# Kernel tuning notes

Hardware: AMD Instinct MI355X
Metric: run time of the kernel (lower is better)

The kernel has to match this reference:

```python
import jax, jax.numpy as jnp
import numpy as np

VOCAB, HIDDEN, LAYERS = 128, 1024, 2
B, T = 128, 512


def setup_inputs() -> dict:
    key = jax.random.key(0)
    ks = jax.random.split(key, 8)
    s0 = 1.0 / np.sqrt(HIDDEN)
    x = jax.random.normal(ks[0], (B, T, VOCAB), dtype=jnp.float32)
    h = jnp.zeros((LAYERS, B, HIDDEN), dtype=jnp.float32)
    c = jnp.zeros((LAYERS, B, HIDDEN), dtype=jnp.float32)
    # LSTM params, gate order (i, f, g, o) concatenated along last dim (4H)
    Wx0 = jax.random.uniform(ks[1], (VOCAB, 4 * HIDDEN), jnp.float32, -s0, s0)
    Wh0 = jax.random.uniform(ks[2], (HIDDEN, 4 * HIDDEN), jnp.float32, -s0, s0)
    b0 = jax.random.uniform(ks[3], (4 * HIDDEN,), jnp.float32, -s0, s0)
    Wx1 = jax.random.uniform(ks[4], (HIDDEN, 4 * HIDDEN), jnp.float32, -s0, s0)
    Wh1 = jax.random.uniform(ks[5], (HIDDEN, 4 * HIDDEN), jnp.float32, -s0, s0)
    b1 = jax.random.uniform(ks[6], (4 * HIDDEN,), jnp.float32, -s0, s0)
    return {"x": x, "h": h, "c": c, "Wx0": Wx0, "Wh0": Wh0, "b0": b0,
            "Wx1": Wx1, "Wh1": Wh1, "b1": b1}


def _lstm_cell(inp, h_prev, c_prev, Wx, Wh, b):
    gates = inp @ Wx + h_prev @ Wh + b            # (B, 4H)
    i, f, g, o = jnp.split(gates, 4, axis=-1)
    i = jax.nn.sigmoid(i)
    f = jax.nn.sigmoid(f)
    g = jnp.tanh(g)
    o = jax.nn.sigmoid(o)
    c_new = f * c_prev + i * g
    h_new = o * jnp.tanh(c_new)
    return h_new, c_new


def reference(x, h, c, Wx0, Wh0, b0, Wx1, Wh1, b1):
    layer_params = [(Wx0, Wh0, b0), (Wx1, Wh1, b1)]

    def step(carry, x_t):
        h_prev, c_prev = carry                    # each (L, B, H)
        inp = x_t                                 # (B, VOCAB)
        hs, cs = [], []
        for l, (Wx, Wh, b) in enumerate(layer_params):
            h_new, c_new = _lstm_cell(inp, h_prev[l], c_prev[l], Wx, Wh, b)
            hs.append(h_new)
            cs.append(c_new)
            inp = h_new
        return (jnp.stack(hs), jnp.stack(cs)), hs[-1]

    xs = jnp.swapaxes(x, 0, 1)                    # (T, B, VOCAB)
    (h_f, c_f), outs = jax.lax.scan(step, (h, c), xs)
    outs = jnp.swapaxes(outs, 0, 1)               # (B, T, H)
    return outs, h_f, c_f
```

## Files before the change

kernel.cpp:

```cpp
#include <hip/hip_runtime.h>

#define VV 128
#define HH 1024
#define BB 128
#define TT 512
#define G4 4096
#define BTH ((size_t)BB * TT * HH)
#define HPAR (4 * 64 * 512)

typedef __attribute__((ext_vector_type(8))) short bf16x8;
typedef __attribute__((ext_vector_type(16))) float f32x16;

__device__ __forceinline__ short f2bf(float f) {
  unsigned u = __float_as_uint(f);
  u = (u + 0x7fffu + ((u >> 16) & 1u)) >> 16;
  return (short)u;
}

__device__ __forceinline__ float fsig(float x) {
  x = fminf(fmaxf(x, -30.f), 30.f);
  float e = __expf(-x);
  return 1.f / (1.f + e);
}
__device__ __forceinline__ float ftanh(float x) {
  x = fminf(fmaxf(x, -15.f), 15.f);
  float e = __expf(-2.f * x);
  return (1.f - e) / (1.f + e);
}


__global__ void conv_x(const float* __restrict__ x, short* __restrict__ xp) {
  const int n = TT * 4 * 8 * 512;
  for (int i = blockIdx.x * blockDim.x + threadIdx.x; i < n; i += gridDim.x * blockDim.x) {
    int e = i & 7, lane = (i >> 3) & 63, kc = (i >> 9) & 7, rb = (i >> 12) & 3, t = i >> 14;
    int row = rb * 32 + (lane & 31);
    int v = kc * 16 + ((lane >> 5) << 3) + e;
    xp[i] = f2bf(x[((size_t)row * TT + t) * VV + v]);
  }
}

__global__ void init_state(const float* __restrict__ h,
                           short* __restrict__ h0p, short* __restrict__ h1p) {
  const int n = 2 * HPAR;
  for (int i = blockIdx.x * blockDim.x + threadIdx.x; i < n; i += gridDim.x * blockDim.x) {
    int inner = i & (HPAR - 1);
    int l = i >> 17;
    int e = i & 7, lane = (i >> 3) & 63, kc = (i >> 9) & 63, rb = (i >> 15) & 3;
    int row = rb * 32 + (lane & 31);
    int j = kc * 16 + ((lane >> 5) << 3) + e;
    short hb = f2bf(h[((size_t)l * BB + row) * HH + j]);
    (l ? h1p : h0p)[HPAR + inner] = hb;
  }
}

__global__ void pack_w(const float* __restrict__ Wx0, const float* __restrict__ Wh0,
                       const float* __restrict__ Wx1, const float* __restrict__ Wh1,
                       short* __restrict__ wp0, short* __restrict__ wp1) {
  const int n0 = 128 * 72 * 512;
  const int n1 = 128 * 128 * 512;
  for (int i = blockIdx.x * blockDim.x + threadIdx.x; i < n0 + n1; i += gridDim.x * blockDim.x) {
    if (i < n0) {
      int cu = i / (72 * 512);
      int rem = i - cu * (72 * 512);
      int kc = rem >> 9, le = rem & 511;
      int lane = le >> 3, e = le & 7;
      int k = kc * 16 + ((lane >> 5) << 3) + e;
      int cl = lane & 31;
      int gcol = (cl >> 3) * HH + cu * 8 + (cl & 7);
      float f = (k < VV) ? Wx0[(size_t)k * G4 + gcol] : Wh0[(size_t)(k - VV) * G4 + gcol];
      wp0[i] = f2bf(f);
    } else {
      int j = i - n0;
      int cu = j >> 16;
      int rem = j & 65535;
      int kc = rem >> 9, le = rem & 511;
      int lane = le >> 3, e = le & 7;
      int k = kc * 16 + ((lane >> 5) << 3) + e;
      int cl = lane & 31;
      int gcol = (cl >> 3) * HH + cu * 8 + (cl & 7);
      float f = (k < HH) ? Wx1[(size_t)k * G4 + gcol] : Wh1[(size_t)(k - HH) * G4 + gcol];
      wp1[j] = f2bf(f);
    }
  }
}

__global__ void pack_b(const float* __restrict__ b0, const float* __restrict__ b1,
                       float* __restrict__ bp, unsigned* __restrict__ slots) {
  int i = blockIdx.x * blockDim.x + threadIdx.x;
  if (i < 2 * 128 * 32) {
    int l = i >> 12;
    int cu = (i >> 5) & 127;
    int cc = i & 31;
    const float* b = l ? b1 : b0;
    bp[i] = b[(cc >> 3) * HH + cu * 8 + (cc & 7)];
  }
  if (i < 512) slots[i] = 0u;
}


template <int NCH>
__device__ __forceinline__ void hgemm(f32x16* acc, const short* pa0, const short* pa1,
                                      const short* __restrict__ pb) {
  constexpr int NG = NCH / 16;
  bf16x8 A[3][16];
#pragma unroll
  for (int g = 0; g < 3; ++g) {
#pragma unroll
    for (int j = 0; j < 16; ++j) {
      const int c = g * 16 + j;
      const short* ap = (c < 64) ? (pa0 + c * 512) : (pa1 + (c - 64) * 512);
      asm volatile("global_load_dwordx4 %0, %1, off sc0 sc1" : "=v"(A[g][j]) : "v"(ap));
    }
  }
#pragma unroll
  for (int g = 0; g < NG; ++g) {
    const int rem = NG - 1 - g;
    if (rem >= 2)      asm volatile("s_waitcnt vmcnt(32)" ::: "memory");
    else if (rem == 1) asm volatile("s_waitcnt vmcnt(16)" ::: "memory");
    else               asm volatile("s_waitcnt vmcnt(0)" ::: "memory");
#pragma unroll
    for (int j = 0; j < 16; ++j)
      asm volatile("" : "+v"(A[g % 3][j]));
#pragma unroll
    for (int j = 0; j < 16; ++j) {
      const int c = g * 16 + j;
      bf16x8 b = *(const bf16x8*)(pb + c * 512);
      acc[j & 3] = __builtin_amdgcn_mfma_f32_32x32x16_bf16(A[g % 3][j], b, acc[j & 3], 0, 0, 0);
    }
    if (g + 3 < NG) {
#pragma unroll
      for (int j = 0; j < 16; ++j) {
        const int c = (g + 3) * 16 + j;
        const short* ap = (c < 64) ? (pa0 + c * 512) : (pa1 + (c - 64) * 512);
        asm volatile("global_load_dwordx4 %0, %1, off sc0 sc1"
                     : "=v"(A[(g + 3) % 3][j]) : "v"(ap));
      }
    }
  }
}

__device__ __forceinline__ void xgemm(f32x16* acc, const short* __restrict__ pax,
                                      const short* __restrict__ pb) {
#pragma unroll
  for (int c = 0; c < 8; ++c) {
    bf16x8 a = *(const bf16x8*)(pax + c * 512);
    bf16x8 b = *(const bf16x8*)(pb + c * 512);
    acc[c & 3] = __builtin_amdgcn_mfma_f32_32x32x16_bf16(a, b, acc[c & 3], 0, 0, 0);
  }
}

__global__ void __launch_bounds__(256, 1) lstm_main(const short* __restrict__ xp,
    short* __restrict__ h0p, short* __restrict__ h1p,
    const short* __restrict__ wp0, const short* __restrict__ wp1,
    const float* __restrict__ bpack, const float* __restrict__ cin,
    float* __restrict__ out, unsigned* __restrict__ slots) {
  __shared__ short wlds[128 * 512];
  unsigned* gdone = slots + 256;
  const int blk = blockIdx.x;
  const int layer = blk >> 7;
  const int cu = blk & 127;
  const int tid = threadIdx.x;
  const int lane = tid & 63;
  const int wave = tid >> 6;

  const int nkc = layer ? 128 : 72;
  const short* wsrc = layer ? (wp1 + (size_t)cu * 128 * 512) : (wp0 + (size_t)cu * 72 * 512);
  for (int i = tid; i < nkc * 64; i += 256)
    ((int4*)wlds)[i] = ((const int4*)wsrc)[i];
  __syncthreads();

  const int col = lane & 31;
  const float bias = bpack[layer * 4096 + cu * 32 + col];
  const int uu = col & 7;
  const bool ewlane = (col < 8);
  const int gcol = cu * 8 + uu;
  const int hi4 = ((lane >> 5) << 2);

  float creg[16], hval[16];
#pragma unroll
  for (int r = 0; r < 16; ++r) {
    int grow = wave * 32 + (r & 3) + ((r >> 2) << 3) + hi4;
    creg[r] = ewlane ? cin[(size_t)layer * BB * HH + (size_t)grow * HH + gcol] : 0.f;
    hval[r] = 0.f;
  }

  const int pst = (wave * 64 + (cu >> 1)) * 512 + ((cu & 1) << 8);

  f32x16 acc[4];
  auto initacc = [&]() {
#pragma unroll
    for (int r = 0; r < 16; ++r) {
      acc[0][r] = bias; acc[1][r] = 0.f; acc[2][r] = 0.f; acc[3][r] = 0.f;
    }
  };

  if (layer == 0) {
    initacc();
    xgemm(acc, xp + ((size_t)(0 * 4 + wave) * 8) * 512 + lane * 8, wlds + lane * 8);
  }

  for (int p = 0; p <= TT; ++p) {
    if (p > 0) {
      const unsigned tgt = (unsigned)p;
      if ((blk & 31) == 0 && tid < 32) {
        for (;;) {
          unsigned v = __hip_atomic_load(&slots[blk + tid],
                                         __ATOMIC_RELAXED, __HIP_MEMORY_SCOPE_AGENT);
          if (__all(v >= tgt)) break;
          __builtin_amdgcn_s_sleep(1);
        }
        if (tid == 0)
          __hip_atomic_store(&gdone[(blk >> 5) << 5], tgt,
                             __ATOMIC_RELAXED, __HIP_MEMORY_SCOPE_AGENT);
      }
      if (tid < 8) {
        for (;;) {
          unsigned v = __hip_atomic_load(&gdone[tid << 5],
                                         __ATOMIC_RELAXED, __HIP_MEMORY_SCOPE_AGENT);
          if (__all(v >= tgt)) break;
          __builtin_amdgcn_s_sleep(1);
        }
      }
      __syncthreads();
    }

    const bool active = layer ? (p >= 1) : (p < TT);
    const int t = layer ? (p - 1) : p;
    if (active) {
      const int parR = (p + 1) & 1;
      if (layer == 0) {
        hgemm<64>(acc, h0p + ((size_t)(parR * 4 + wave) * 64) * 512 + lane * 8,
                  h0p, wlds + 8 * 512 + lane * 8);
      } else {
        initacc();
        hgemm<128>(acc, h0p + ((size_t)(parR * 4 + wave) * 64) * 512 + lane * 8,
                   h1p + ((size_t)((p & 1) * 4 + wave) * 64) * 512 + lane * 8,
                   wlds + lane * 8);
      }
      f32x16 accf = (acc[0] + acc[1]) + (acc[2] + acc[3]);
      short* hp = layer ? (h1p + (size_t)((p + 1) & 1) * HPAR)
                        : (h0p + (size_t)(p & 1) * HPAR);
#pragma unroll
      for (int r = 0; r < 16; ++r) {
        float a0 = accf[r];
        float nl = (col >= 16 && col < 24) ? ftanh(a0) : fsig(a0);
        float f_ = __shfl_xor(nl, 8);
        float g_ = __shfl_xor(nl, 16);
        float o_ = __shfl_xor(nl, 24);
        const int rloc = (r & 3) + ((r >> 2) << 3) + hi4;
        const int grow = wave * 32 + rloc;
        float hnew = 0.f;
        if (ewlane) {
          float cnew = f_ * creg[r] + nl * g_;
          creg[r] = cnew;
          hnew = o_ * ftanh(cnew);
          hval[r] = hnew;
        }
        unsigned hb = (unsigned short)f2bf(hnew);
        unsigned pb2 = (unsigned)__shfl_xor((int)hb, 1);
        if (ewlane) {
          if (t == TT - 1) {
            out[BTH + (size_t)layer * BB * HH + (size_t)grow * HH + gcol] = hnew;
            out[BTH + (size_t)(2 + layer) * BB * HH + (size_t)grow * HH + gcol] = creg[r];
          }
          if (!(uu & 1)) {
            unsigned dw = hb | (pb2 << 16);
            __hip_atomic_store((unsigned*)(hp + pst + rloc * 8 + uu), dw,
                               __ATOMIC_RELAXED, __HIP_MEMORY_SCOPE_AGENT);
          }
        }
      }
    }

    if (p == TT) {
      if (layer && active && ewlane) {
#pragma unroll
        for (int r = 0; r < 16; ++r) {
          const int rloc = (r & 3) + ((r >> 2) << 3) + hi4;
          const int grow = wave * 32 + rloc;
          out[(size_t)grow * TT * HH + (size_t)t * HH + gcol] = hval[r];
        }
      }
      break;
    }

    __syncthreads();
    if (tid == 0)
      __hip_atomic_store(&slots[blk], (unsigned)(p + 1),
                         __ATOMIC_RELAXED, __HIP_MEMORY_SCOPE_AGENT);

    if (layer == 0) {
      if (p + 1 < TT) {
        initacc();
        xgemm(acc, xp + ((size_t)((p + 1) * 4 + wave) * 8) * 512 + lane * 8, wlds + lane * 8);
      }
    } else if (active && ewlane) {
#pragma unroll
      for (int r = 0; r < 16; ++r) {
        const int rloc = (r & 3) + ((r >> 2) << 3) + hi4;
        const int grow = wave * 32 + rloc;
        out[(size_t)grow * TT * HH + (size_t)t * HH + gcol] = hval[r];
      }
    }
  }
}


extern "C" void kernel_launch(void* const* d_in, const int* in_sizes, int n_in,
                              void* d_out, int out_size, void* d_ws, size_t ws_size,
                              hipStream_t stream) {
  const float* x   = (const float*)d_in[0];
  const float* h   = (const float*)d_in[1];
  const float* c   = (const float*)d_in[2];
  const float* Wx0 = (const float*)d_in[3];
  const float* Wh0 = (const float*)d_in[4];
  const float* b0  = (const float*)d_in[5];
  const float* Wx1 = (const float*)d_in[6];
  const float* Wh1 = (const float*)d_in[7];
  const float* b1  = (const float*)d_in[8];
  float* out = (float*)d_out;

  char* ws = (char*)d_ws;
  short* xp  = (short*)ws;
  short* h0p = (short*)(ws + 16777216);
  short* h1p = (short*)(ws + 17301504);
  short* wp0 = (short*)(ws + 17825792);
  short* wp1 = (short*)(ws + 27262976);
  float* bp  = (float*)(ws + 44040192);
  unsigned* slots = (unsigned*)(ws + 44072960);

  hipLaunchKernelGGL(conv_x,     dim3(2048), dim3(256), 0, stream, x, xp);
  hipLaunchKernelGGL(init_state, dim3(512),  dim3(256), 0, stream, h, h0p, h1p);
  hipLaunchKernelGGL(pack_w,     dim3(4096), dim3(256), 0, stream, Wx0, Wh0, Wx1, Wh1, wp0, wp1);
  hipLaunchKernelGGL(pack_b,     dim3(32),   dim3(256), 0, stream, b0, b1, bp, slots);

  hipLaunchKernelGGL(lstm_main, dim3(256), dim3(256), 0, stream,
                     xp, h0p, h1p, wp0, wp1, bp, c, out, slots);
}
```

Before: 6.390 ms.

## Use a 256-slot hidden-state ring buffer to allow non-bypassing cached loads

Replaces the double-buffered hidden-state exchange with a 256-entry ring of buffers indexed by a scrambled timestep hash. Because each slot is rewritten only once every 256 steps, the hgemm reads drop the sc1 system-coherence bit and may hit in cache instead of bypassing it. The ring path needs about 178MB of workspace and is chosen only when ws_size is large enough, otherwise the old path runs. It relies on stale cache lines for a slot being evicted within 256 steps, which is a correctness risk.

```diff
diff --git a/kernel.cpp b/kernel.cpp
--- a/kernel.cpp
+++ b/kernel.cpp
@@ -7,6 +7,7 @@
 #define G4 4096
 #define BTH ((size_t)BB * TT * HH)
 #define HPAR (4 * 64 * 512)
+#define RING 256
 
 typedef __attribute__((ext_vector_type(8))) short bf16x8;
 typedef __attribute__((ext_vector_type(16))) float f32x16;
@@ -26,6 +27,10 @@
   x = fminf(fmaxf(x, -15.f), 15.f);
   float e = __expf(-2.f * x);
   return (1.f - e) / (1.f + e);
+}
+
+__device__ __forceinline__ unsigned eidx(int t) {
+  return ((unsigned)(t + 1) * 37u) & (RING - 1);
 }
 
 
@@ -40,7 +45,7 @@
 }
 
 __global__ void init_state(const float* __restrict__ h,
-                           short* __restrict__ h0p, short* __restrict__ h1p) {
+                           short* __restrict__ h0dst, short* __restrict__ h1dst) {
   const int n = 2 * HPAR;
   for (int i = blockIdx.x * blockDim.x + threadIdx.x; i < n; i += gridDim.x * blockDim.x) {
     int inner = i & (HPAR - 1);
@@ -49,7 +54,7 @@
     int row = rb * 32 + (lane & 31);
     int j = kc * 16 + ((lane >> 5) << 3) + e;
     short hb = f2bf(h[((size_t)l * BB + row) * HH + j]);
-    (l ? h1p : h0p)[HPAR + inner] = hb;
+    (l ? h1dst : h0dst)[inner] = hb;
   }
 }
 
@@ -98,7 +103,7 @@
 }
 
 
-template <int NCH>
+template <int NCH, bool COH>
 __device__ __forceinline__ void hgemm(f32x16* acc, const short* pa0, const short* pa1,
                                       const short* __restrict__ pb) {
   constexpr int NG = NCH / 16;
@@ -109,7 +114,10 @@
     for (int j = 0; j < 16; ++j) {
       const int c = g * 16 + j;
       const short* ap = (c < 64) ? (pa0 + c * 512) : (pa1 + (c - 64) * 512);
-      asm volatile("global_load_dwordx4 %0, %1, off sc0 sc1" : "=v"(A[g][j]) : "v"(ap));
+      if constexpr (COH)
+        asm volatile("global_load_dwordx4 %0, %1, off sc0 sc1" : "=v"(A[g][j]) : "v"(ap));
+      else
+        asm volatile("global_load_dwordx4 %0, %1, off sc0" : "=v"(A[g][j]) : "v"(ap));
     }
   }
 #pragma unroll
@@ -132,8 +140,12 @@
       for (int j = 0; j < 16; ++j) {
         const int c = (g + 3) * 16 + j;
         const short* ap = (c < 64) ? (pa0 + c * 512) : (pa1 + (c - 64) * 512);
-        asm volatile("global_load_dwordx4 %0, %1, off sc0 sc1"
-                     : "=v"(A[(g + 3) % 3][j]) : "v"(ap));
+        if constexpr (COH)
+          asm volatile("global_load_dwordx4 %0, %1, off sc0 sc1"
+                       : "=v"(A[(g + 3) % 3][j]) : "v"(ap));
+        else
+          asm volatile("global_load_dwordx4 %0, %1, off sc0"
+                       : "=v"(A[(g + 3) % 3][j]) : "v"(ap));
       }
     }
   }
@@ -149,8 +161,9 @@
   }
 }
 
+template <bool RINGM>
 __global__ void __launch_bounds__(256, 1) lstm_main(const short* __restrict__ xp,
-    short* __restrict__ h0p, short* __restrict__ h1p,
+    short* __restrict__ h0b, short* __restrict__ h1b,
     const short* __restrict__ wp0, const short* __restrict__ wp1,
     const float* __restrict__ bpack, const float* __restrict__ cin,
     float* __restrict__ out, unsigned* __restrict__ slots) {
@@ -185,6 +198,7 @@
   }
 
   const int pst = (wave * 64 + (cu >> 1)) * 512 + ((cu & 1) << 8);
+  const int wv64 = wave * 64 * 512 + lane * 8;
 
   f32x16 acc[4];
   auto initacc = [&]() {
@@ -227,19 +241,29 @@
     const bool active = layer ? (p >= 1) : (p < TT);
     const int t = layer ? (p - 1) : p;
     if (active) {
-      const int parR = (p + 1) & 1;
+      const short *ra0, *ra1;
+      if constexpr (RINGM) {
+        ra0 = h0b + (size_t)eidx(p - 1) * HPAR + wv64;
+        ra1 = h1b + (size_t)eidx(p - 2) * HPAR + wv64;
+      } else {
+        const int parR = (p + 1) & 1;
+        ra0 = h0b + (size_t)parR * HPAR + wv64;
+        ra1 = h1b + (size_t)(p & 1) * HPAR + wv64;
+      }
       if (layer == 0) {
-        hgemm<64>(acc, h0p + ((size_t)(parR * 4 + wave) * 64) * 512 + lane * 8,
-                  h0p, wlds + 8 * 512 + lane * 8);
+        hgemm<64, !RINGM>(acc, ra0, ra0, wlds + 8 * 512 + lane * 8);
       } else {
         initacc();
-        hgemm<128>(acc, h0p + ((size_t)(parR * 4 + wave) * 64) * 512 + lane * 8,
-                   h1p + ((size_t)((p & 1) * 4 + wave) * 64) * 512 + lane * 8,
-                   wlds + lane * 8);
+        hgemm<128, !RINGM>(acc, ra0, ra1, wlds + lane * 8);
       }
       f32x16 accf = (acc[0] + acc[1]) + (acc[2] + acc[3]);
-      short* hp = layer ? (h1p + (size_t)((p + 1) & 1) * HPAR)
-                        : (h0p + (size_t)(p & 1) * HPAR);
+      short* hp;
+      if constexpr (RINGM)
+        hp = layer ? (h1b + (size_t)eidx(p - 1) * HPAR)
+                   : (h0b + (size_t)eidx(p) * HPAR);
+      else
+        hp = layer ? (h1b + (size_t)((p + 1) & 1) * HPAR)
+                   : (h0b + (size_t)(p & 1) * HPAR);
 #pragma unroll
       for (int r = 0; r < 16; ++r) {
         float a0 = accf[r];
@@ -322,18 +346,31 @@
 
   char* ws = (char*)d_ws;
   short* xp  = (short*)ws;
-  short* h0p = (short*)(ws + 16777216);
-  short* h1p = (short*)(ws + 17301504);
-  short* wp0 = (short*)(ws + 17825792);
-  short* wp1 = (short*)(ws + 27262976);
-  float* bp  = (float*)(ws + 44040192);
-  unsigned* slots = (unsigned*)(ws + 44072960);
+  short* wp0 = (short*)(ws + 16777216);
+  short* wp1 = (short*)(ws + 26214400);
+  float* bp  = (float*)(ws + 42991616);
+  unsigned* slots = (unsigned*)(ws + 43024384);
+  short* h0p = (short*)(ws + 43026432);
+  short* h1p = (short*)(ws + 43550720);
+  short* h0r = (short*)(ws + 44075008);
+  short* h1r = (short*)(ws + 111183872);
+  const size_t need_ring = 178292736;
+
+  const bool ring = (ws_size >= need_ring);
+  short* h0 = ring ? h0r : h0p;
+  short* h1 = ring ? h1r : h1p;
+  short* h0ini = ring ? h0r : (h0p + HPAR);
+  short* h1ini = ring ? h1r : (h1p + HPAR);
 
   hipLaunchKernelGGL(conv_x,     dim3(2048), dim3(256), 0, stream, x, xp);
-  hipLaunchKernelGGL(init_state, dim3(512),  dim3(256), 0, stream, h, h0p, h1p);
+  hipLaunchKernelGGL(init_state, dim3(512),  dim3(256), 0, stream, h, h0ini, h1ini);
   hipLaunchKernelGGL(pack_w,     dim3(4096), dim3(256), 0, stream, Wx0, Wh0, Wx1, Wh1, wp0, wp1);
   hipLaunchKernelGGL(pack_b,     dim3(32),   dim3(256), 0, stream, b0, b1, bp, slots);
 
-  hipLaunchKernelGGL(lstm_main, dim3(256), dim3(256), 0, stream,
-                     xp, h0p, h1p, wp0, wp1, bp, c, out, slots);
-}
+  if (ring)
+    hipLaunchKernelGGL((lstm_main<true>), dim3(256), dim3(256), 0, stream,
+                       xp, h0, h1, wp0, wp1, bp, c, out, slots);
+  else
+    hipLaunchKernelGGL((lstm_main<false>), dim3(256), dim3(256), 0, stream,
+                       xp, h0, h1, wp0, wp1, bp, c, out, slots);
+}
```

New measurement: 6.379 ms. About the same (-0.2%).
